# Optimization experiments

Measured on AMD Instinct MI355X. Metric: run time of the kernel, lower is better.

## Reference

```python
import math
import jax, jax.numpy as jnp
import numpy as np

B, C_IN, H, W = 32, 96, 64, 64
OUT = 128
EXC = int(OUT * 0.8)   # 102 excitatory channels
INH = OUT - EXC        # 26 inhibitory channels
K = 5
PAD = 2                # kernel//2 so all stages keep spatial size


def _sm_kernel(kernel_size=5, sigma_e=1.2, sigma_i=1.4):
    c = kernel_size // 2
    xx, yy = np.meshgrid(np.arange(kernel_size), np.arange(kernel_size), indexing='ij')
    xx = xx.astype(np.float32) - c
    yy = yy.astype(np.float32) - c
    ge = np.exp(-(xx ** 2 + yy ** 2) / (2 * sigma_e ** 2))
    gi = np.exp(-(xx ** 2 + yy ** 2) / (2 * sigma_i ** 2))
    dog = ge / (2 * math.pi * sigma_e ** 2) - gi / (2 * math.pi * sigma_i ** 2)
    dog = dog / dog[c, c]
    return jnp.asarray(dog[None, None], dtype=jnp.float32)  # [1,1,K,K]


def setup_inputs() -> dict:
    key = jax.random.key(0)
    k1, k2, k3, k4 = jax.random.split(key, 4)
    wr = 25.0 / math.sqrt(C_IN * K * K)
    x = jax.random.normal(k1, (B, C_IN, H, W), jnp.float32)
    w_ee = wr * jnp.abs(jax.random.normal(k2, (EXC, C_IN, K, K), jnp.float32))
    w_ei = wr * jnp.abs(jax.random.normal(k3, (INH, EXC, K, K), jnp.float32))
    w_ie = -wr * jnp.abs(jax.random.normal(k4, (EXC, INH, K, K), jnp.float32))
    return {"x": x, "w_ee": w_ee, "w_ei": w_ei, "w_ie": w_ie, "sm_kernel": _sm_kernel()}


def _reflect_pad(x, p):
    if p == 0:
        return x
    return jnp.pad(x, ((0, 0), (0, 0), (p, p), (p, p)), mode='reflect')


def _conv(x, w, pad=0, groups=1):
    return jax.lax.conv_general_dilated(
        x, w, window_strides=(1, 1), padding=[(pad, pad), (pad, pad)],
        dimension_numbers=('NCHW', 'OIHW', 'NCHW'), feature_group_count=groups)


def _forward(x, w_ee, w_ei, w_ie, sm_kernel):
    y_e = _conv(_reflect_pad(x, PAD), w_ee)                 # [B,EXC,H,W], act=Identity
    y_i = jax.nn.relu(_conv(_reflect_pad(y_e, PAD), w_ei))  # [B,INH,H,W]
    y_ie = _conv(_reflect_pad(y_i, PAD), w_ie)              # [B,EXC,H,W]
    y = y_e + y_ie
    # depthwise surround-modulation conv (zero padding, as in F.conv2d)
    w_sm = jnp.tile(sm_kernel, (EXC, 1, 1, 1))              # [EXC,1,K,K]
    y = _conv(y, w_sm, pad=K // 2, groups=EXC)
    return y, y_e, y_i


def reference(x, w_ee, w_ei, w_ie, sm_kernel):
    y, y_e, y_i = _forward(x, w_ee, w_ei, w_ie, sm_kernel)

    # --- hard WTA masks (winner channel per (b,h,w) position) ---
    win_e = jnp.argmax(y_e, axis=1)                                        # [B,H,W]
    mask_e = (jnp.arange(EXC)[None, :, None, None] == win_e[:, None]).astype(y_e.dtype)
    y_wta_e = y_e * mask_e
    win_i = jnp.argmax(jnp.abs(y_i), axis=1)
    mask_i = (jnp.arange(INH)[None, :, None, None] == win_i[:, None]).astype(y_i.dtype)
    y_wta_i = y_i * mask_i

    # --- transpose-conv outer-product trick; with same-size feature maps the
    # conv collapses to a 1x1 full correlation over (b,h,w) -> einsum ---
    yx_ee = jnp.einsum('bchw,behw->ec', x, y_wta_e)[:, :, None, None]      # [EXC,C_IN,1,1]
    yx_ei = jnp.einsum('behw,bihw->ie', y_wta_e, y_wta_i)[:, :, None, None]  # [INH,EXC,1,1]
    yx_ie = jnp.einsum('bihw,behw->ei', y_wta_i, y)[:, :, None, None]      # [EXC,INH,1,1]

    yu_e = jnp.sum(y_wta_e, axis=(0, 2, 3))[:, None, None, None]           # [EXC,1,1,1]
    yu_i = jnp.sum(jnp.abs(y_wta_i), axis=(0, 2, 3))[:, None, None, None]  # [INH,1,1,1]

    upd_ee = yx_ee - yu_e * w_ee   # broadcasts to [EXC,C_IN,K,K]
    upd_ei = yx_ei - yu_i * w_ei
    upd_ie = yx_ie - yu_e * w_ie
    upd_ee = upd_ee / (jnp.abs(upd_ee).max() + 1e-8)
    upd_ei = upd_ei / (jnp.abs(upd_ei).max() + 1e-8)
    upd_ie = upd_ie / (jnp.abs(upd_ie).max() + 1e-8)

    return (y, upd_ee, upd_ei, upd_ie)
```

## Files before the change

kernel.cpp:

```cpp
#include <hip/hip_runtime.h>

#define B_    32
#define CIN_  96
#define EXC_  102
#define INH_  26
#define HH    64
#define WW    64
#define HW_   4096
#define NPOS  (B_*HW_)
#define EEPAD 97
#define NPART 512
#define NEE   (EXC_*CIN_ + EXC_)
#define NIE   (EXC_*INH_)
#define N1U   (EXC_*CIN_*25)
#define N2U   (INH_*EXC_*25)
#define N3U   (EXC_*INH_*25)

typedef short bf8 __attribute__((ext_vector_type(8)));
typedef float f32x4 __attribute__((ext_vector_type(4)));

__device__ __forceinline__ int refl(int i) {
    if (i < 0) i = -i;
    if (i > 63) i = 126 - i;
    return i;
}

__device__ __forceinline__ short f2bf(float f) {
    unsigned u = __float_as_uint(f);
    return (short)((u + 0x7fffu + ((u >> 16) & 1u)) >> 16);
}

__global__ __launch_bounds__(256) void pack_all(
    const float* __restrict__ w_ee, const float* __restrict__ w_ei,
    const float* __restrict__ w_ie, const float* __restrict__ x,
    short* __restrict__ wdst, short* __restrict__ xdst,
    float* __restrict__ zreg)
{
    const int blk = blockIdx.x;
    if (blk < 1800) {
        int gi = blk*256 + threadIdx.x;
        if (gi >= 460800) return;
        const float* src; int N, C, NPAD, CPAD; int idx;
        if (gi < 268800)      { src = w_ee; N = 102; C = 96;  NPAD = 112; CPAD = 96;  idx = gi; }
        else if (gi < 371200) { src = w_ei; N = 26;  C = 102; NPAD = 32;  CPAD = 128; idx = gi - 268800; }
        else                  { src = w_ie; N = 102; C = 26;  NPAD = 112; CPAD = 32;  idx = gi - 371200; }
        int tap = idx / (NPAD*CPAD);
        int rem = idx - tap*(NPAD*CPAD);
        int n = rem / CPAD, c = rem - n*CPAD;
        float f = (n < N && c < C) ? src[((size_t)n*C + c)*25 + tap] : 0.f;
        wdst[gi] = f2bf(f);
    } else if (blk < 3848) {
        int bb = blk - 1800;
        int b = bb >> 6, bx = bb & 63;
        const int pos = bx*64 + (threadIdx.x & 63);
        const int cg0 = threadIdx.x >> 6;
        for (int cg = cg0; cg < 96/8; cg += 4) {
            bf8 v;
#pragma unroll
            for (int j = 0; j < 8; ++j)
                v[j] = f2bf(x[((size_t)b*CIN_ + cg*8 + j)*HW_ + pos]);
            *(bf8*)(&xdst[((size_t)b*HW_ + pos)*96 + cg*8]) = v;
        }
    } else {
        for (int i = threadIdx.x; i < INH_*EXC_ + INH_ + 3; i += 256) zreg[i] = 0.f;
    }
}

template<int C, int CPAD>
__global__ __launch_bounds__(256) void pack_nhwc(
    const float* __restrict__ src, short* __restrict__ dst)
{
    const int b = blockIdx.z;
    const int pos = blockIdx.x*64 + (threadIdx.x & 63);
    const int cg0 = threadIdx.x >> 6;
    for (int cg = cg0; cg < CPAD/8; cg += 4) {
        bf8 v;
#pragma unroll
        for (int j = 0; j < 8; ++j) {
            int c = cg*8 + j;
            float f = (c < C) ? src[((size_t)b*C + c)*HW_ + pos] : 0.f;
            v[j] = f2bf(f);
        }
        *(bf8*)(&dst[((size_t)b*HW_ + pos)*CPAD + cg*8]) = v;
    }
}

template<int CPAD, int NPAD, int NT, int COUT, int NCHUNK,
         bool RELU, bool ADDIN, bool WFLOAT, int OCPAD, bool WTA>
__global__ __launch_bounds__(256, 2) void conv_mfma(
    const short* __restrict__ src, const short* __restrict__ wgt,
    const float* __restrict__ addin, float* __restrict__ out,
    short* __restrict__ nhwc_out, int* __restrict__ win,
    float* __restrict__ val)
{
    __shared__ __align__(16) short sA[400*40];
    const int t  = threadIdx.x;
    const int bx = blockIdx.x;
    const int b  = blockIdx.z;
    const int h0 = (bx >> 2) * 16;
    const int w0 = (bx &  3) * 16;
    const int lane = t & 63;
    const int wv = t >> 6;
    const int nh = lane & 15;
    const int q  = lane >> 4;

    int goff[7], loff[7];
#pragma unroll
    for (int s = 0; s < 7; ++s) {
        int i = t + 256*s;
        if (i < 1600) {
            int rec = i >> 2, seg = i & 3;
            int lh = rec / 20, lw = rec - lh*20;
            int gh = refl(h0 - 2 + lh), gw = refl(w0 - 2 + lw);
            goff[s] = (b*HW_ + gh*WW + gw) * CPAD + seg*8;
            loff[s] = rec*40 + seg*8;
        } else { goff[s] = 0; loff[s] = -1; }
    }

    f32x4 acc[4][NT];
#pragma unroll
    for (int mt = 0; mt < 4; ++mt)
#pragma unroll
        for (int nt = 0; nt < NT; ++nt) {
            f32x4 z = {0.f, 0.f, 0.f, 0.f};
            acc[mt][nt] = z;
        }

    int abase[4];
#pragma unroll
    for (int mt = 0; mt < 4; ++mt)
        abase[mt] = ((wv*4 + mt)*20 + nh)*40 + q*8;

    for (int ck = 0; ck < NCHUNK; ++ck) {
        const int c0 = ck*32;
        __syncthreads();
#pragma unroll
        for (int s = 0; s < 7; ++s)
            if (loff[s] >= 0)
                *(bf8*)(&sA[loff[s]]) = *(const bf8*)(&src[goff[s] + c0]);
        __syncthreads();
        const short* wch = wgt + c0 + nh*CPAD + q*8;
        for (int dh = 0; dh < 5; ++dh) {
#pragma unroll
            for (int dw = 0; dw < 5; ++dw) {
                const int tap = dh*5 + dw;
                bf8 bfr[NT];
#pragma unroll
                for (int nt = 0; nt < NT; ++nt)
                    bfr[nt] = *(const bf8*)(&wch[(size_t)(tap*NPAD + nt*16)*CPAD]);
                bf8 afr[4];
#pragma unroll
                for (int mt = 0; mt < 4; ++mt)
                    afr[mt] = *(const bf8*)(&sA[abase[mt] + (dh*20 + dw)*40]);
#pragma unroll
                for (int mt = 0; mt < 4; ++mt)
#pragma unroll
                    for (int nt = 0; nt < NT; ++nt)
                        acc[mt][nt] = __builtin_amdgcn_mfma_f32_16x16x32_bf16(
                            afr[mt], bfr[nt], acc[mt][nt], 0, 0, 0);
            }
        }
    }

#pragma unroll
    for (int mt = 0; mt < 4; ++mt) {
        const int rowi = h0 + wv*4 + mt;
#pragma unroll
        for (int nt = 0; nt < NT; ++nt) {
            const int chn = nt*16 + nh;
            if (WFLOAT && chn < COUT) {
                size_t obase = ((size_t)(b*COUT + chn))*HW_ + rowi*WW + w0 + q*4;
#pragma unroll
                for (int r = 0; r < 4; ++r) {
                    float v = acc[mt][nt][r];
                    if (RELU) v = fmaxf(v, 0.f);
                    if (ADDIN) v += addin[obase + r];
                    out[obase + r] = v;
                }
            }
            if (OCPAD > 0) {
#pragma unroll
                for (int r = 0; r < 4; ++r) {
                    float v = acc[mt][nt][r];
                    if (RELU) v = fmaxf(v, 0.f);
                    int pos = rowi*WW + w0 + q*4 + r;
                    nhwc_out[((size_t)b*HW_ + pos)*OCPAD + chn] = f2bf(v);
                }
            }
        }
        if (OCPAD > NT*16) {
#pragma unroll
            for (int r = 0; r < 4; ++r) {
                int pos = rowi*WW + w0 + q*4 + r;
                for (int ct = NT*16 + nh; ct < OCPAD; ct += 16)
                    nhwc_out[((size_t)b*HW_ + pos)*OCPAD + ct] = 0;
            }
        }
        if (WTA) {
#pragma unroll
            for (int r = 0; r < 4; ++r) {
                float bv = -3.402823e38f; int bc = 0;
#pragma unroll
                for (int nt = 0; nt < NT; ++nt) {
                    const int chn = nt*16 + nh;
                    float v = acc[mt][nt][r];
                    if (RELU) v = fmaxf(v, 0.f);
                    if (chn < COUT && v > bv) { bv = v; bc = chn; }
                }
#pragma unroll
                for (int off = 1; off < 16; off <<= 1) {
                    float ov = __shfl_xor(bv, off);
                    int   oc = __shfl_xor(bc, off);
                    if (ov > bv || (ov == bv && oc < bc)) { bv = ov; bc = oc; }
                }
                if (nh == 0) {
                    int p = b*HW_ + rowi*WW + w0 + q*4 + r;
                    win[p] = bc; val[p] = bv;
                }
            }
        }
    }
}

__global__ __launch_bounds__(256) void smconv_v2(
    const float* __restrict__ in, const float* __restrict__ sm,
    float* __restrict__ out)
{
    __shared__ __align__(16) float sx[36*36];
    const int tid = threadIdx.x;
    const int tile = blockIdx.x;
    const int e = blockIdx.y;
    const int b = blockIdx.z;
    const int h0 = (tile >> 1) * 32, w0 = (tile & 1) * 32;
    const int r  = tid >> 3;
    const int cg = (tid & 7) * 4;
    const float* inc = in + ((size_t)(b*EXC_ + e))*HW_;
#pragma unroll
    for (int it = 0; it < 6; ++it) {
        int i = tid + it*256;
        if (i < 1296) {
            int lh = i / 36, lw = i - lh*36;
            int gh = h0 - 2 + lh, gw = w0 - 2 + lw;
            float v = 0.f;
            if (gh >= 0 && gh < HH && gw >= 0 && gw < WW) v = inc[gh*WW + gw];
            sx[i] = v;
        }
    }
    __syncthreads();
    float a0 = 0.f, a1 = 0.f, a2 = 0.f, a3 = 0.f;
#pragma unroll
    for (int kh = 0; kh < 5; ++kh) {
        const float4* rowp = (const float4*)(sx + (r + kh)*36 + cg);
        float4 v0 = rowp[0], v1 = rowp[1];
        float xv[8] = {v0.x, v0.y, v0.z, v0.w, v1.x, v1.y, v1.z, v1.w};
#pragma unroll
        for (int kw = 0; kw < 5; ++kw) {
            float wv = sm[kh*5 + kw];
            a0 = fmaf(xv[kw+0], wv, a0);
            a1 = fmaf(xv[kw+1], wv, a1);
            a2 = fmaf(xv[kw+2], wv, a2);
            a3 = fmaf(xv[kw+3], wv, a3);
        }
    }
    size_t oidx = ((size_t)(b*EXC_ + e))*HW_ + (h0 + r)*WW + w0 + cg;
    *(float4*)(out + oidx) = make_float4(a0, a1, a2, a3);
}

__global__ __launch_bounds__(256) void scatter_all_kernel(
    const float* __restrict__ x, const float* __restrict__ y,
    const int* __restrict__ win_e, const float* __restrict__ val_e,
    const int* __restrict__ win_i, const float* __restrict__ val_i,
    float* __restrict__ yx_ei, float* __restrict__ yu_i,
    float* __restrict__ parts_ee, float* __restrict__ parts_ie)
{
    __shared__ float s_yx[EXC_*EEPAD];
    __shared__ float s_yu[EXC_];
    __shared__ float s_ei[INH_*EXC_ + INH_];
    __shared__ float s_ie[EXC_*INH_];
    for (int i = threadIdx.x; i < EXC_*EEPAD; i += 256) s_yx[i] = 0.f;
    if (threadIdx.x < EXC_) s_yu[threadIdx.x] = 0.f;
    for (int i = threadIdx.x; i < INH_*EXC_ + INH_; i += 256) s_ei[i] = 0.f;
    for (int i = threadIdx.x; i < EXC_*INH_; i += 256) s_ie[i] = 0.f;
    __syncthreads();

    int p = blockIdx.x * 256 + threadIdx.x;
    int b = p >> 12, hw = p & 4095;
    int we = win_e[p]; float ve = val_e[p];
    int wi = win_i[p]; float vi = val_i[p];

    atomicAdd(&s_ei[wi*EXC_ + we], ve*vi);
    atomicAdd(&s_ei[INH_*EXC_ + wi], fabsf(vi));

    atomicAdd(&s_yu[we], ve);
    {
        const float* xb = x + ((size_t)b*CIN_)*HW_ + hw;
        float* row = s_yx + we*EEPAD;
        for (int c = 0; c < CIN_; ++c)
            atomicAdd(&row[c], ve * xb[(size_t)c*HW_]);
    }

    if (vi != 0.f) {
        const float* yb = y + ((size_t)b*EXC_)*HW_ + hw;
        for (int e = 0; e < EXC_; ++e)
            atomicAdd(&s_ie[e*INH_ + wi], vi * yb[(size_t)e*HW_]);
    }
    __syncthreads();

    float* dee = parts_ee + (size_t)blockIdx.x * NEE;
    for (int i = threadIdx.x; i < EXC_*CIN_; i += 256) {
        int e = i / CIN_, c = i - e*CIN_;
        dee[i] = s_yx[e*EEPAD + c];
    }
    if (threadIdx.x < EXC_) dee[EXC_*CIN_ + threadIdx.x] = s_yu[threadIdx.x];
    for (int i = threadIdx.x; i < INH_*EXC_ + INH_; i += 256) {
        float v = s_ei[i];
        if (v != 0.f) {
            if (i < INH_*EXC_) atomicAdd(&yx_ei[i], v);
            else               atomicAdd(&yu_i[i - INH_*EXC_], v);
        }
    }
    float* die = parts_ie + (size_t)blockIdx.x * NIE;
    for (int i = threadIdx.x; i < EXC_*INH_; i += 256) die[i] = s_ie[i];
}

__global__ __launch_bounds__(256) void reduce_all_kernel(
    const float* __restrict__ parts_ee, const float* __restrict__ parts_ie,
    float* __restrict__ yx_ee, float* __restrict__ yx_ie)
{
    __shared__ float s[256];
    int col = blockIdx.x*64 + (threadIdx.x & 63);
    int g = threadIdx.x >> 6;
    const float* P; float* D; int n, i;
    if (col < NEE) { P = parts_ee; D = yx_ee; n = NEE; i = col; }
    else           { P = parts_ie; D = yx_ie; n = NIE; i = col - NEE; }
    float a = 0.f;
    if (col < NEE + NIE) {
        for (int j = g*(NPART/4); j < (g+1)*(NPART/4); ++j)
            a += P[(size_t)j*n + i];
    }
    s[threadIdx.x] = a;
    __syncthreads();
    if (threadIdx.x < 64 && col < NEE + NIE)
        D[i] = s[threadIdx.x] + s[threadIdx.x+64] + s[threadIdx.x+128] + s[threadIdx.x+192];
}

__global__ __launch_bounds__(256) void upd_absmax3(
    const float* __restrict__ yx_ee, const float* __restrict__ yu_e,
    const float* __restrict__ w_ee,
    const float* __restrict__ yx_ei, const float* __restrict__ yu_i,
    const float* __restrict__ w_ei,
    const float* __restrict__ yx_ie, const float* __restrict__ w_ie,
    unsigned int* __restrict__ amax)
{
    float m0 = 0.f, m1 = 0.f, m2 = 0.f;
    for (int idx = blockIdx.x*256 + threadIdx.x; idx < N1U + N2U + N3U;
         idx += gridDim.x*256) {
        if (idx < N1U) {
            int ec = idx / 25; int e = ec / CIN_;
            m0 = fmaxf(m0, fabsf(yx_ee[ec] - yu_e[e]*w_ee[idx]));
        } else if (idx < N1U + N2U) {
            int j = idx - N1U; int ec = j / 25; int e = ec / EXC_;
            m1 = fmaxf(m1, fabsf(yx_ei[ec] - yu_i[e]*w_ei[j]));
        } else {
            int j = idx - N1U - N2U; int ec = j / 25; int e = ec / INH_;
            m2 = fmaxf(m2, fabsf(yx_ie[ec] - yu_e[e]*w_ie[j]));
        }
    }
    __shared__ unsigned int s0, s1, s2;
    if (threadIdx.x == 0) { s0 = 0u; s1 = 0u; s2 = 0u; }
    __syncthreads();
    atomicMax(&s0, __float_as_uint(m0));
    atomicMax(&s1, __float_as_uint(m1));
    atomicMax(&s2, __float_as_uint(m2));
    __syncthreads();
    if (threadIdx.x == 0) {
        atomicMax(&amax[0], s0);
        atomicMax(&amax[1], s1);
        atomicMax(&amax[2], s2);
    }
}

__global__ __launch_bounds__(256) void upd_write3(
    const float* __restrict__ yx_ee, const float* __restrict__ yu_e,
    const float* __restrict__ w_ee,
    const float* __restrict__ yx_ei, const float* __restrict__ yu_i,
    const float* __restrict__ w_ei,
    const float* __restrict__ yx_ie, const float* __restrict__ w_ie,
    const unsigned int* __restrict__ amax,
    float* __restrict__ out_ee, float* __restrict__ out_ei,
    float* __restrict__ out_ie)
{
    int idx = blockIdx.x*256 + threadIdx.x;
    if (idx >= N1U + N2U + N3U) return;
    if (idx < N1U) {
        int ec = idx / 25; int e = ec / CIN_;
        float v = yx_ee[ec] - yu_e[e]*w_ee[idx];
        out_ee[idx] = v / (__uint_as_float(amax[0]) + 1e-8f);
    } else if (idx < N1U + N2U) {
        int j = idx - N1U; int ec = j / 25; int e = ec / EXC_;
        float v = yx_ei[ec] - yu_i[e]*w_ei[j];
        out_ei[j] = v / (__uint_as_float(amax[1]) + 1e-8f);
    } else {
        int j = idx - N1U - N2U; int ec = j / 25; int e = ec / INH_;
        float v = yx_ie[ec] - yu_e[e]*w_ie[j];
        out_ie[j] = v / (__uint_as_float(amax[2]) + 1e-8f);
    }
}

extern "C" void kernel_launch(void* const* d_in, const int* in_sizes, int n_in,
                              void* d_out, int out_size, void* d_ws, size_t ws_size,
                              hipStream_t stream)
{
    const float* x    = (const float*)d_in[0];
    const float* w_ee = (const float*)d_in[1];
    const float* w_ei = (const float*)d_in[2];
    const float* w_ie = (const float*)d_in[3];
    const float* smk  = (const float*)d_in[4];
    float* out = (float*)d_out;

    const size_t SZ_YE   = (size_t)B_*EXC_*HW_;
    const size_t SZ_YEBF = (size_t)B_*HW_*128;
    const size_t SZ_XBF  = (size_t)B_*HW_*96;
    const size_t SZ_W    = 460800;
    const size_t need_direct =
        SZ_YE*4 + SZ_YEBF*2 + SZ_XBF*2 + SZ_W*2 + (size_t)NPOS*16 + 16000*4;
    const bool direct = (ws_size >= need_direct);

    float* y_e  = (float*)d_ws;
    short* yebf; short* R;
    if (direct) {
        yebf = (short*)(y_e + SZ_YE);
        R    = yebf + SZ_YEBF;
    } else {
        yebf = nullptr;
        R    = (short*)(y_e + SZ_YE);
    }
    short* yibf = direct ? R : R;
    short* bigR = direct ? R : (R + (size_t)B_*HW_*32);
    short* wee  = direct ? (R + SZ_XBF) : (bigR + (size_t)16777216);
    short* wei  = wee + 268800;
    short* wie  = wei + 102400;
    int*   win_e = (int*)(wie + 89600);
    float* val_e = (float*)(win_e + NPOS);
    int*   win_i = (int*)(val_e + NPOS);
    float* val_i = (float*)(win_i + NPOS);
    float* yx_ee = val_i + NPOS;
    float* yu_e  = yx_ee + EXC_*CIN_;
    float* yx_ie = yu_e + EXC_;
    float* yx_ei = yx_ie + EXC_*INH_;
    float* yu_i  = yx_ei + INH_*EXC_;
    unsigned int* amax = (unsigned int*)(yu_i + INH_);
    float* parts_ee = y_e;
    float* parts_ie = parts_ee + (size_t)NPART*NEE;

    pack_all<<<3849, 256, 0, stream>>>(w_ee, w_ei, w_ie, x, wee, bigR, yx_ei);

    if (direct) {
        conv_mfma<96, 112, 7, EXC_, 3, false, false, true, 128, true>
            <<<dim3(16, 1, B_), 256, 0, stream>>>(bigR, wee, nullptr, y_e, yebf,
                                                  win_e, val_e);
        conv_mfma<128, 32, 2, INH_, 4, true, false, false, 32, true>
            <<<dim3(16, 1, B_), 256, 0, stream>>>(yebf, wei, nullptr, nullptr,
                                                  yibf, win_i, val_i);
        conv_mfma<32, 112, 7, EXC_, 1, false, true, true, 0, false>
            <<<dim3(16, 1, B_), 256, 0, stream>>>(yibf, wie, y_e, y_e, nullptr,
                                                  nullptr, nullptr);
    } else {
        conv_mfma<96, 112, 7, EXC_, 3, false, false, true, 0, true>
            <<<dim3(16, 1, B_), 256, 0, stream>>>(bigR, wee, nullptr, y_e, nullptr,
                                                  win_e, val_e);
        pack_nhwc<EXC_, 128><<<dim3(64, 1, B_), 256, 0, stream>>>(y_e, bigR);
        conv_mfma<128, 32, 2, INH_, 4, true, false, false, 32, true>
            <<<dim3(16, 1, B_), 256, 0, stream>>>(bigR, wei, nullptr, nullptr,
                                                  yibf, win_i, val_i);
        conv_mfma<32, 112, 7, EXC_, 1, false, true, true, 0, false>
            <<<dim3(16, 1, B_), 256, 0, stream>>>(yibf, wie, y_e, y_e, nullptr,
                                                  nullptr, nullptr);
    }

    smconv_v2<<<dim3(4, EXC_, B_), 256, 0, stream>>>(y_e, smk, out);

    scatter_all_kernel<<<NPART, 256, 0, stream>>>(x, out, win_e, val_e, win_i,
                                                  val_i, yx_ei, yu_i,
                                                  parts_ee, parts_ie);

    reduce_all_kernel<<<(NEE + NIE + 63)/64, 256, 0, stream>>>(
        parts_ee, parts_ie, yx_ee, yx_ie);

    upd_absmax3<<<480, 256, 0, stream>>>(yx_ee, yu_e, w_ee, yx_ei, yu_i, w_ei,
                                         yx_ie, w_ie, amax);
    float* out_ee = out + (size_t)B_*EXC_*HW_;
    float* out_ei = out_ee + N1U;
    float* out_ie = out_ei + N2U;
    upd_write3<<<(N1U + N2U + N3U + 255)/256, 256, 0, stream>>>(
        yx_ee, yu_e, w_ee, yx_ei, yu_i, w_ei, yx_ie, w_ie, amax,
        out_ee, out_ei, out_ie);
}
```

Measured before the change: 551.5 us.

## Split scatter kernel into two kernels and halve channel work per thread

Replaces the fused scatter kernel with two separate kernels, one for the x·y_e correlation and one for the e-i and i-e correlations. Each block now covers 128 positions and splits the channel loop between two thread halves, so the partial count doubles to 1024. This gives more parallelism and shorter serial atomic loops per thread, and each kernel needs less shared memory. In exchange the partial buffers become twice as large, which adds write traffic and more work in the reduce kernel, and there is one extra launch.

```diff
diff --git a/kernel.cpp b/kernel.cpp
--- a/kernel.cpp
+++ b/kernel.cpp
@@ -9,7 +9,7 @@
 #define HW_   4096
 #define NPOS  (B_*HW_)
 #define EEPAD 97
-#define NPART 512
+#define NPART 1024
 #define NEE   (EXC_*CIN_ + EXC_)
 #define NIE   (EXC_*INH_)
 #define N1U   (EXC_*CIN_*25)
@@ -266,52 +266,62 @@
     *(float4*)(out + oidx) = make_float4(a0, a1, a2, a3);
 }
 
-__global__ __launch_bounds__(256) void scatter_all_kernel(
-    const float* __restrict__ x, const float* __restrict__ y,
-    const int* __restrict__ win_e, const float* __restrict__ val_e,
-    const int* __restrict__ win_i, const float* __restrict__ val_i,
-    float* __restrict__ yx_ei, float* __restrict__ yu_i,
-    float* __restrict__ parts_ee, float* __restrict__ parts_ie)
+__global__ __launch_bounds__(256) void scatter_ee_kernel(
+    const float* __restrict__ x, const int* __restrict__ win_e,
+    const float* __restrict__ val_e, float* __restrict__ parts)
 {
     __shared__ float s_yx[EXC_*EEPAD];
     __shared__ float s_yu[EXC_];
+    for (int i = threadIdx.x; i < EXC_*EEPAD; i += 256) s_yx[i] = 0.f;
+    if (threadIdx.x < EXC_) s_yu[threadIdx.x] = 0.f;
+    __syncthreads();
+    const int pos_i = threadIdx.x & 127;
+    const int half  = threadIdx.x >> 7;
+    int p = blockIdx.x * 128 + pos_i;
+    int b = p >> 12, hw = p & 4095;
+    int wi = win_e[p]; float v = val_e[p];
+    if (half == 0) atomicAdd(&s_yu[wi], v);
+    const float* xb = x + ((size_t)b*CIN_ + half*48)*HW_ + hw;
+    float* row = s_yx + wi*EEPAD + half*48;
+    for (int c = 0; c < 48; ++c)
+        atomicAdd(&row[c], v * xb[(size_t)c*HW_]);
+    __syncthreads();
+    float* dst = parts + (size_t)blockIdx.x * NEE;
+    for (int i = threadIdx.x; i < EXC_*CIN_; i += 256) {
+        int e = i / CIN_, c = i - e*CIN_;
+        dst[i] = s_yx[e*EEPAD + c];
+    }
+    if (threadIdx.x < EXC_) dst[EXC_*CIN_ + threadIdx.x] = s_yu[threadIdx.x];
+}
+
+__global__ __launch_bounds__(256) void scatter_iei_kernel(
+    const float* __restrict__ y, const int* __restrict__ win_e,
+    const float* __restrict__ val_e, const int* __restrict__ win_i,
+    const float* __restrict__ val_i, float* __restrict__ yx_ei,
+    float* __restrict__ yu_i, float* __restrict__ parts)
+{
     __shared__ float s_ei[INH_*EXC_ + INH_];
     __shared__ float s_ie[EXC_*INH_];
-    for (int i = threadIdx.x; i < EXC_*EEPAD; i += 256) s_yx[i] = 0.f;
-    if (threadIdx.x < EXC_) s_yu[threadIdx.x] = 0.f;
     for (int i = threadIdx.x; i < INH_*EXC_ + INH_; i += 256) s_ei[i] = 0.f;
     for (int i = threadIdx.x; i < EXC_*INH_; i += 256) s_ie[i] = 0.f;
     __syncthreads();
-
-    int p = blockIdx.x * 256 + threadIdx.x;
+    const int pos_i = threadIdx.x & 127;
+    const int half  = threadIdx.x >> 7;
+    int p = blockIdx.x * 128 + pos_i;
     int b = p >> 12, hw = p & 4095;
-    int we = win_e[p]; float ve = val_e[p];
     int wi = win_i[p]; float vi = val_i[p];
-
-    atomicAdd(&s_ei[wi*EXC_ + we], ve*vi);
-    atomicAdd(&s_ei[INH_*EXC_ + wi], fabsf(vi));
-
-    atomicAdd(&s_yu[we], ve);
-    {
-        const float* xb = x + ((size_t)b*CIN_)*HW_ + hw;
-        float* row = s_yx + we*EEPAD;
-        for (int c = 0; c < CIN_; ++c)
-            atomicAdd(&row[c], ve * xb[(size_t)c*HW_]);
-    }
-
+    if (half == 0) {
+        int we = win_e[p]; float ve = val_e[p];
+        atomicAdd(&s_ei[wi*EXC_ + we], ve*vi);
+        atomicAdd(&s_ei[INH_*EXC_ + wi], fabsf(vi));
+    }
     if (vi != 0.f) {
-        const float* yb = y + ((size_t)b*EXC_)*HW_ + hw;
-        for (int e = 0; e < EXC_; ++e)
-            atomicAdd(&s_ie[e*INH_ + wi], vi * yb[(size_t)e*HW_]);
-    }
-    __syncthreads();
-
-    float* dee = parts_ee + (size_t)blockIdx.x * NEE;
-    for (int i = threadIdx.x; i < EXC_*CIN_; i += 256) {
-        int e = i / CIN_, c = i - e*CIN_;
-        dee[i] = s_yx[e*EEPAD + c];
-    }
-    if (threadIdx.x < EXC_) dee[EXC_*CIN_ + threadIdx.x] = s_yu[threadIdx.x];
+        const float* yb = y + ((size_t)b*EXC_ + half*51)*HW_ + hw;
+        float* se = s_ie + half*51*INH_ + wi;
+        for (int e = 0; e < 51; ++e)
+            atomicAdd(&se[e*INH_], vi * yb[(size_t)e*HW_]);
+    }
+    __syncthreads();
     for (int i = threadIdx.x; i < INH_*EXC_ + INH_; i += 256) {
         float v = s_ei[i];
         if (v != 0.f) {
@@ -319,8 +329,8 @@
             else               atomicAdd(&yu_i[i - INH_*EXC_], v);
         }
     }
-    float* die = parts_ie + (size_t)blockIdx.x * NIE;
-    for (int i = threadIdx.x; i < EXC_*INH_; i += 256) die[i] = s_ie[i];
+    float* dst = parts + (size_t)blockIdx.x * NIE;
+    for (int i = threadIdx.x; i < EXC_*INH_; i += 256) dst[i] = s_ie[i];
 }
 
 __global__ __launch_bounds__(256) void reduce_all_kernel(
@@ -480,9 +490,9 @@
 
     smconv_v2<<<dim3(4, EXC_, B_), 256, 0, stream>>>(y_e, smk, out);
 
-    scatter_all_kernel<<<NPART, 256, 0, stream>>>(x, out, win_e, val_e, win_i,
-                                                  val_i, yx_ei, yu_i,
-                                                  parts_ee, parts_ie);
+    scatter_ee_kernel<<<NPART, 256, 0, stream>>>(x, win_e, val_e, parts_ee);
+    scatter_iei_kernel<<<NPART, 256, 0, stream>>>(out, win_e, val_e, win_i,
+                                                  val_i, yx_ei, yu_i, parts_ie);
 
     reduce_all_kernel<<<(NEE + NIE + 63)/64, 256, 0, stream>>>(
         parts_ee, parts_ie, yx_ee, yx_ie);
```

Measured after the change: 580.1 us. 5.2% more time.

## Remap scatter kernel threads to channels instead of positions for conflict-free LDS atomics

Applied to the files above, without the earlier changes.

Rewrites the scatter kernel so that each thread owns one input channel (first 128 threads) or one excitatory channel (last 128 threads) and loops over the block's 256 positions. Before, each thread owned one position and looped over channels. Each thread now streams its channel row with float4 loads and adds into a distinct shared-memory column. This is meant to cut LDS atomic contention, where many lanes previously hit the same winner row, and to make the global reads of x and y coalesced per row. In exchange, the winner and value arrays are re-read by every thread, and the loops become longer and serial, using only 96 or 102 of each 128-thread half.

```diff
diff --git a/kernel.cpp b/kernel.cpp
--- a/kernel.cpp
+++ b/kernel.cpp
@@ -8,7 +8,6 @@
 #define WW    64
 #define HW_   4096
 #define NPOS  (B_*HW_)
-#define EEPAD 97
 #define NPART 512
 #define NEE   (EXC_*CIN_ + EXC_)
 #define NIE   (EXC_*INH_)
@@ -273,44 +272,71 @@
     float* __restrict__ yx_ei, float* __restrict__ yu_i,
     float* __restrict__ parts_ee, float* __restrict__ parts_ie)
 {
-    __shared__ float s_yx[EXC_*EEPAD];
+    __shared__ float s_yx[EXC_*CIN_];
     __shared__ float s_yu[EXC_];
+    __shared__ float s_ie[EXC_*27];
     __shared__ float s_ei[INH_*EXC_ + INH_];
-    __shared__ float s_ie[EXC_*INH_];
-    for (int i = threadIdx.x; i < EXC_*EEPAD; i += 256) s_yx[i] = 0.f;
+    for (int i = threadIdx.x; i < EXC_*CIN_; i += 256) s_yx[i] = 0.f;
     if (threadIdx.x < EXC_) s_yu[threadIdx.x] = 0.f;
+    for (int i = threadIdx.x; i < EXC_*27; i += 256) s_ie[i] = 0.f;
     for (int i = threadIdx.x; i < INH_*EXC_ + INH_; i += 256) s_ei[i] = 0.f;
-    for (int i = threadIdx.x; i < EXC_*INH_; i += 256) s_ie[i] = 0.f;
     __syncthreads();
 
-    int p = blockIdx.x * 256 + threadIdx.x;
-    int b = p >> 12, hw = p & 4095;
-    int we = win_e[p]; float ve = val_e[p];
-    int wi = win_i[p]; float vi = val_i[p];
-
-    atomicAdd(&s_ei[wi*EXC_ + we], ve*vi);
-    atomicAdd(&s_ei[INH_*EXC_ + wi], fabsf(vi));
-
-    atomicAdd(&s_yu[we], ve);
+    const int p0  = blockIdx.x * 256;
+    const int b   = p0 >> 12;
+    const int hw0 = p0 & 4095;
+    const int t   = threadIdx.x;
+
     {
-        const float* xb = x + ((size_t)b*CIN_)*HW_ + hw;
-        float* row = s_yx + we*EEPAD;
-        for (int c = 0; c < CIN_; ++c)
-            atomicAdd(&row[c], ve * xb[(size_t)c*HW_]);
-    }
-
-    if (vi != 0.f) {
-        const float* yb = y + ((size_t)b*EXC_)*HW_ + hw;
-        for (int e = 0; e < EXC_; ++e)
-            atomicAdd(&s_ie[e*INH_ + wi], vi * yb[(size_t)e*HW_]);
+        int p = p0 + t;
+        int we = win_e[p]; float ve = val_e[p];
+        int wi = win_i[p]; float vi = val_i[p];
+        atomicAdd(&s_ei[wi*EXC_ + we], ve*vi);
+        atomicAdd(&s_ei[INH_*EXC_ + wi], fabsf(vi));
+    }
+
+    if (t < 128) {
+        const int c = t;
+        if (c < CIN_) {
+            const float* xrow = x + ((size_t)b*CIN_ + c)*HW_ + hw0;
+            const float4* xr4 = (const float4*)xrow;
+#pragma unroll 4
+            for (int p4 = 0; p4 < 64; ++p4) {
+                float4 xv = xr4[p4];
+#pragma unroll
+                for (int j = 0; j < 4; ++j) {
+                    int pp = p0 + p4*4 + j;
+                    int we = win_e[pp]; float ve = val_e[pp];
+                    float xj = (j == 0) ? xv.x : (j == 1) ? xv.y : (j == 2) ? xv.z : xv.w;
+                    atomicAdd(&s_yx[we*CIN_ + c], ve*xj);
+                    if (c == 0) atomicAdd(&s_yu[we], ve);
+                }
+            }
+        }
+    } else {
+        const int e = t - 128;
+        if (e < EXC_) {
+            const float* yrow = y + ((size_t)b*EXC_ + e)*HW_ + hw0;
+            const float4* yr4 = (const float4*)yrow;
+#pragma unroll 4
+            for (int p4 = 0; p4 < 64; ++p4) {
+                float4 yv = yr4[p4];
+#pragma unroll
+                for (int j = 0; j < 4; ++j) {
+                    int pp = p0 + p4*4 + j;
+                    int wi = win_i[pp]; float vi = val_i[pp];
+                    if (vi != 0.f) {
+                        float yj = (j == 0) ? yv.x : (j == 1) ? yv.y : (j == 2) ? yv.z : yv.w;
+                        atomicAdd(&s_ie[e*27 + wi], vi*yj);
+                    }
+                }
+            }
+        }
     }
     __syncthreads();
 
     float* dee = parts_ee + (size_t)blockIdx.x * NEE;
-    for (int i = threadIdx.x; i < EXC_*CIN_; i += 256) {
-        int e = i / CIN_, c = i - e*CIN_;
-        dee[i] = s_yx[e*EEPAD + c];
-    }
+    for (int i = threadIdx.x; i < EXC_*CIN_; i += 256) dee[i] = s_yx[i];
     if (threadIdx.x < EXC_) dee[EXC_*CIN_ + threadIdx.x] = s_yu[threadIdx.x];
     for (int i = threadIdx.x; i < INH_*EXC_ + INH_; i += 256) {
         float v = s_ei[i];
@@ -320,7 +346,10 @@
         }
     }
     float* die = parts_ie + (size_t)blockIdx.x * NIE;
-    for (int i = threadIdx.x; i < EXC_*INH_; i += 256) die[i] = s_ie[i];
+    for (int i = threadIdx.x; i < EXC_*INH_; i += 256) {
+        int e = i / INH_, ii = i - e*INH_;
+        die[i] = s_ie[e*27 + ii];
+    }
 }
 
 __global__ __launch_bounds__(256) void reduce_all_kernel(
```

Measured after the change: 542.5 us. About the same (-1.6%).
